# Performance work log

Measured on AMD Instinct MI355X. Metric: run time of the kernel, lower is better.

## Reference

```python
import jax, jax.numpy as jnp
import numpy as np

B, L = 512, 200
WORD_V, PATH_V = 100000, 200000
E, D = 128, 384


def setup_inputs() -> dict:
    key = jax.random.key(0)
    ks = jax.random.split(key, 10)
    inp = {
        "x_s1": jax.random.randint(ks[0], (B, L), 0, WORD_V),
        "path1": jax.random.randint(ks[1], (B, L), 0, PATH_V),
        "x_t1": jax.random.randint(ks[2], (B, L), 0, WORD_V),
        "x_s2": jax.random.randint(ks[3], (B, L), 0, WORD_V),
        "path2": jax.random.randint(ks[4], (B, L), 0, PATH_V),
        "x_t2": jax.random.randint(ks[5], (B, L), 0, WORD_V),
        # learned parameters
        "word_emb": jax.random.normal(ks[6], (WORD_V, E), dtype=jnp.float32) * 0.02,
        "path_emb": jax.random.normal(ks[7], (PATH_V, E), dtype=jnp.float32) * 0.02,
        "W_fc": jax.random.normal(ks[8], (D, 3 * E), dtype=jnp.float32) * (1.0 / np.sqrt(3 * E)),  # nn.Linear weight [out, in], no bias
        "attn": jax.random.uniform(ks[9], (D, 1), dtype=jnp.float32),
    }
    return inp


def _extract(xs, path, xt, word_emb, path_emb, W_fc, attn):
    # gather + concat -> [B, L, 3E]
    ctx = jnp.concatenate([word_emb[xs], path_emb[path], word_emb[xt]], axis=-1)
    # linear (no bias, dropout is identity at eval) + tanh -> [B, L, D]
    h = jnp.tanh(jnp.einsum('blf,df->bld', ctx, W_fc))
    # attention scores [B, L, 1]; the zeros mask in the original is a no-op
    scores = jnp.einsum('bld,do->blo', h, attn)
    a = jax.nn.softmax(scores, axis=1)
    code_vec = jnp.sum(h * a, axis=1)  # [B, D]
    return code_vec, a


def reference(x_s1, path1, x_t1, x_s2, path2, x_t2, word_emb, path_emb, W_fc, attn):
    cv1, _ = _extract(x_s1, path1, x_t1, word_emb, path_emb, W_fc, attn)
    cv2, _ = _extract(x_s2, path2, x_t2, word_emb, path_emb, W_fc, attn)
    return (cv1, cv2)
```

## Files before the change

kernel.cpp:

```cpp
#include <hip/hip_runtime.h>
#include <hip/hip_bf16.h>

#define B_N   512
#define L_N   200
#define E_N   128
#define D_N   384
#define K_N   384
#define M_PAD 208
#define MT_N  13
#define NT_W  3
#define NWAVE 8
#define KSTEP 12
#define STR   136

typedef __bf16 v8bf  __attribute__((ext_vector_type(8)));
typedef float  v4f   __attribute__((ext_vector_type(4)));
typedef unsigned int v4u __attribute__((ext_vector_type(4)));

__device__ __forceinline__ unsigned short f2bf(float f) {
    union { __bf16 b; unsigned short u; } cv;
    cv.b = (__bf16)f;
    return cv.u;
}

__device__ __forceinline__ float fast_tanh(float x) {
    float e = __expf(2.f * x);
    return 1.f - 2.f / (e + 1.f);
}

__global__ void pack_w(const float* __restrict__ W, unsigned short* __restrict__ Wp) {
    int gid  = blockIdx.x * 256 + threadIdx.x;
    int lane = gid & 63;
    int u    = gid >> 6;
    int nt   = u % 3;
    int wv   = (u / 3) & 7;
    int kk   = u / 24;
    int c    = lane & 15;
    int quad = lane >> 4;
    int n    = wv * 48 + nt * 16 + c;
    int k0   = kk * 32 + quad * 8;
    const float* src = W + n * K_N + k0;
    ushort4 lo, hi;
    lo.x = f2bf(src[0]); lo.y = f2bf(src[1]); lo.z = f2bf(src[2]); lo.w = f2bf(src[3]);
    hi.x = f2bf(src[4]); hi.y = f2bf(src[5]); hi.z = f2bf(src[6]); hi.w = f2bf(src[7]);
    ushort4* dst = (ushort4*)(Wp + (size_t)gid * 8);
    dst[0] = lo;
    dst[1] = hi;
}

__global__ __launch_bounds__(512, 2)
void code2vec_fused(const int* __restrict__ xs1, const int* __restrict__ ph1,
                    const int* __restrict__ xt1,
                    const int* __restrict__ xs2, const int* __restrict__ ph2,
                    const int* __restrict__ xt2,
                    const float* __restrict__ wemb, const float* __restrict__ pemb,
                    const unsigned short* __restrict__ Wp,
                    const float* __restrict__ attn,
                    float* __restrict__ out)
{
    const int tid  = threadIdx.x;
    const int wv   = tid >> 6;
    const int lane = tid & 63;
    const int quad = lane >> 4;
    const int c    = lane & 15;
    const int b    = blockIdx.x;
    const int pass = blockIdx.y;

    const int* xs = pass ? xs2 : xs1;
    const int* ph = pass ? ph2 : ph1;
    const int* xt = pass ? xt2 : xt1;

    __shared__ unsigned short Alds[M_PAD * STR];
    __shared__ float sp[NWAVE][M_PAD];
    __shared__ float alds[M_PAD];
    __shared__ int   ilds[3 * L_N];

    if (tid < L_N) {
        ilds[tid]           = xs[b * L_N + tid];
        ilds[L_N + tid]     = ph[b * L_N + tid];
        ilds[2 * L_N + tid] = xt[b * L_N + tid];
    }

    v4f acc[MT_N][NT_W];
    #pragma unroll
    for (int i = 0; i < MT_N; ++i)
        #pragma unroll
        for (int j = 0; j < NT_W; ++j)
            acc[i][j] = (v4f){0.f, 0.f, 0.f, 0.f};

    const v4u* wp4 = (const v4u*)Wp;

    for (int seg = 0; seg < 3; ++seg) {
        const float* ebase = (seg == 1) ? pemb : wemb;
        const int*   idxp  = &ilds[seg * L_N];

        __syncthreads();

        #pragma unroll
        for (int i = 0; i < 7; ++i) {
            int u = i * 512 + tid;
            if (u < M_PAD * 16) {
                int m = u >> 4, jj = u & 15;
                ushort4 lo, hi;
                if (m < L_N) {
                    const float* src = ebase + (size_t)idxp[m] * E_N + jj * 8;
                    const float4 f0 = *(const float4*)(src);
                    const float4 f1 = *(const float4*)(src + 4);
                    lo.x = f2bf(f0.x); lo.y = f2bf(f0.y); lo.z = f2bf(f0.z); lo.w = f2bf(f0.w);
                    hi.x = f2bf(f1.x); hi.y = f2bf(f1.y); hi.z = f2bf(f1.z); hi.w = f2bf(f1.w);
                } else {
                    lo.x = lo.y = lo.z = lo.w = 0;
                    hi.x = hi.y = hi.z = hi.w = 0;
                }
                ushort4* dst = (ushort4*)&Alds[m * STR + jj * 8];
                dst[0] = lo;
                dst[1] = hi;
            }
        }
        __syncthreads();

        #pragma unroll
        for (int t = 0; t < 4; ++t) {
            const int kk = seg * 4 + t;
            v8bf bfrag[NT_W];
            #pragma unroll
            for (int nt = 0; nt < NT_W; ++nt) {
                v4u raw = wp4[((kk * NWAVE + wv) * NT_W + nt) * 64 + lane];
                bfrag[nt] = __builtin_bit_cast(v8bf, raw);
            }
            #pragma unroll
            for (int mt = 0; mt < MT_N; ++mt) {
                v8bf afrag = *(const v8bf*)&Alds[(mt * 16 + c) * STR + t * 32 + quad * 8];
                #pragma unroll
                for (int nt = 0; nt < NT_W; ++nt)
                    acc[mt][nt] = __builtin_amdgcn_mfma_f32_16x16x32_bf16(afrag, bfrag[nt], acc[mt][nt], 0, 0, 0);
            }
        }
    }

    float an[NT_W];
    #pragma unroll
    for (int nt = 0; nt < NT_W; ++nt) an[nt] = attn[wv * 48 + nt * 16 + c];

    #pragma unroll
    for (int mt = 0; mt < MT_N; ++mt) {
        #pragma unroll
        for (int r = 0; r < 4; ++r) {
            float sv = 0.f;
            #pragma unroll
            for (int nt = 0; nt < NT_W; ++nt) {
                float h = fast_tanh(acc[mt][nt][r]);
                acc[mt][nt][r] = h;
                sv += h * an[nt];
            }
            sv += __shfl_xor(sv, 1);
            sv += __shfl_xor(sv, 2);
            sv += __shfl_xor(sv, 4);
            sv += __shfl_xor(sv, 8);
            if (c == 0) sp[wv][mt * 16 + quad * 4 + r] = sv;
        }
    }
    __syncthreads();

    if (tid < M_PAD) {
        float s = 0.f;
        #pragma unroll
        for (int w2 = 0; w2 < NWAVE; ++w2) s += sp[w2][tid];
        alds[tid] = s;
    }
    __syncthreads();

    if (wv == 0) {
        float v0 = alds[lane];
        float v1 = alds[64 + lane];
        float v2 = alds[128 + lane];
        bool  has3 = (192 + lane) < L_N;
        float v3 = has3 ? alds[192 + lane] : -1e30f;
        float mx = fmaxf(fmaxf(v0, v1), fmaxf(v2, v3));
        #pragma unroll
        for (int off = 32; off > 0; off >>= 1) mx = fmaxf(mx, __shfl_xor(mx, off));
        float e0 = __expf(v0 - mx);
        float e1 = __expf(v1 - mx);
        float e2 = __expf(v2 - mx);
        float e3 = has3 ? __expf(v3 - mx) : 0.f;
        float z = e0 + e1 + e2 + e3;
        #pragma unroll
        for (int off = 32; off > 0; off >>= 1) z += __shfl_xor(z, off);
        float inv = 1.f / z;
        alds[lane]       = e0 * inv;
        alds[64 + lane]  = e1 * inv;
        alds[128 + lane] = e2 * inv;
        if (192 + lane < M_PAD) alds[192 + lane] = e3 * inv;
    }
    __syncthreads();

    float* outp = out + (size_t)pass * B_N * D_N + (size_t)b * D_N;
    #pragma unroll
    for (int nt = 0; nt < NT_W; ++nt) {
        float cv = 0.f;
        #pragma unroll
        for (int mt = 0; mt < MT_N; ++mt) {
            #pragma unroll
            for (int r = 0; r < 4; ++r)
                cv += alds[mt * 16 + quad * 4 + r] * acc[mt][nt][r];
        }
        cv += __shfl_xor(cv, 16);
        cv += __shfl_xor(cv, 32);
        if (quad == 0) outp[wv * 48 + nt * 16 + c] = cv;
    }
}

extern "C" void kernel_launch(void* const* d_in, const int* in_sizes, int n_in,
                              void* d_out, int out_size, void* d_ws, size_t ws_size,
                              hipStream_t stream) {
    unsigned short* Wp = (unsigned short*)d_ws;
    pack_w<<<72, 256, 0, stream>>>((const float*)d_in[8], Wp);
    dim3 grid(B_N, 2, 1);
    code2vec_fused<<<grid, 512, 0, stream>>>(
        (const int*)d_in[0], (const int*)d_in[1], (const int*)d_in[2],
        (const int*)d_in[3], (const int*)d_in[4], (const int*)d_in[5],
        (const float*)d_in[6], (const float*)d_in[7],
        Wp, (const float*)d_in[9],
        (float*)d_out);
}
```

Baseline: 358.8 us.

## Split sequence into row chunks with online softmax to cut registers and LDS

The fused kernel now processes the 200 positions in three chunks (80/64/64 rows) instead of holding all 13 M-tiles of accumulators at once. It uses a flash-style running max/sum softmax to combine the chunks. This shrinks per-thread accumulators and the LDS tile, so launch bounds can rise to 4 blocks per CU for more occupancy. The cost is three extra gather/GEMM passes with more barriers, and the W fragments are reloaded for each chunk.

Result: slower. 386.9 us (+7.8%).

```diff
diff --git a/kernel.cpp b/kernel.cpp
--- a/kernel.cpp
+++ b/kernel.cpp
@@ -1,17 +1,12 @@
 #include <hip/hip_runtime.h>
 #include <hip/hip_bf16.h>
 
-#define B_N   512
-#define L_N   200
-#define E_N   128
-#define D_N   384
-#define K_N   384
-#define M_PAD 208
-#define MT_N  13
-#define NT_W  3
-#define NWAVE 8
-#define KSTEP 12
-#define STR   136
+#define B_N 512
+#define L_N 200
+#define E_N 128
+#define D_N 384
+#define K_N 384
+#define STR 136
 
 typedef __bf16 v8bf  __attribute__((ext_vector_type(8)));
 typedef float  v4f   __attribute__((ext_vector_type(4)));
@@ -22,7 +17,6 @@
     cv.b = (__bf16)f;
     return cv.u;
 }
-
 __device__ __forceinline__ float fast_tanh(float x) {
     float e = __expf(2.f * x);
     return 1.f - 2.f / (e + 1.f);
@@ -32,31 +26,26 @@
     int gid  = blockIdx.x * 256 + threadIdx.x;
     int lane = gid & 63;
     int u    = gid >> 6;
-    int nt   = u % 3;
-    int wv   = (u / 3) & 7;
+    int gn   = u % 24;
     int kk   = u / 24;
-    int c    = lane & 15;
-    int quad = lane >> 4;
-    int n    = wv * 48 + nt * 16 + c;
-    int k0   = kk * 32 + quad * 8;
-    const float* src = W + n * K_N + k0;
+    int c    = lane & 15, quad = lane >> 4;
+    const float* src = W + (gn * 16 + c) * K_N + kk * 32 + quad * 8;
     ushort4 lo, hi;
     lo.x = f2bf(src[0]); lo.y = f2bf(src[1]); lo.z = f2bf(src[2]); lo.w = f2bf(src[3]);
     hi.x = f2bf(src[4]); hi.y = f2bf(src[5]); hi.z = f2bf(src[6]); hi.w = f2bf(src[7]);
     ushort4* dst = (ushort4*)(Wp + (size_t)gid * 8);
-    dst[0] = lo;
-    dst[1] = hi;
-}
-
-__global__ __launch_bounds__(512, 2)
-void code2vec_fused(const int* __restrict__ xs1, const int* __restrict__ ph1,
-                    const int* __restrict__ xt1,
-                    const int* __restrict__ xs2, const int* __restrict__ ph2,
-                    const int* __restrict__ xt2,
-                    const float* __restrict__ wemb, const float* __restrict__ pemb,
-                    const unsigned short* __restrict__ Wp,
-                    const float* __restrict__ attn,
-                    float* __restrict__ out)
+    dst[0] = lo; dst[1] = hi;
+}
+
+__global__ __launch_bounds__(512, 4)
+void c2v_fused(const int* __restrict__ xs1, const int* __restrict__ ph1,
+               const int* __restrict__ xt1,
+               const int* __restrict__ xs2, const int* __restrict__ ph2,
+               const int* __restrict__ xt2,
+               const float* __restrict__ wemb, const float* __restrict__ pemb,
+               const unsigned short* __restrict__ Wp,
+               const float* __restrict__ attn,
+               float* __restrict__ out)
 {
     const int tid  = threadIdx.x;
     const int wv   = tid >> 6;
@@ -70,40 +59,49 @@
     const int* ph = pass ? ph2 : ph1;
     const int* xt = pass ? xt2 : xt1;
 
-    __shared__ unsigned short Alds[M_PAD * STR];
-    __shared__ float sp[NWAVE][M_PAD];
-    __shared__ float alds[M_PAD];
-    __shared__ int   ilds[3 * L_N];
-
-    if (tid < L_N) {
-        ilds[tid]           = xs[b * L_N + tid];
-        ilds[L_N + tid]     = ph[b * L_N + tid];
-        ilds[2 * L_N + tid] = xt[b * L_N + tid];
+    __shared__ unsigned short Alds[80 * STR];
+    __shared__ float sp[8][80];
+    __shared__ float alds[130];
+    __shared__ int   ilds[3 * 208];
+
+    for (int u = tid; u < 624; u += 512) {
+        int s = u / 208, g = u - s * 208;
+        const int* tab = (s == 0) ? xs : (s == 1) ? ph : xt;
+        ilds[u] = (g < L_N) ? tab[b * L_N + g] : 0;
     }
 
-    v4f acc[MT_N][NT_W];
-    #pragma unroll
-    for (int i = 0; i < MT_N; ++i)
+    const float an0 = attn[(wv * 3 + 0) * 16 + c];
+    const float an1 = attn[(wv * 3 + 1) * 16 + c];
+    const float an2 = attn[(wv * 3 + 2) * 16 + c];
+
+    float o0 = 0.f, o1 = 0.f, o2 = 0.f;
+    float Mrun = -1e30f, Zrun = 0.f;
+
+    const v4u* wp4 = (const v4u*)Wp;
+
+    for (int chunk = 0; chunk < 3; ++chunk) {
+        const int mtn  = (chunk == 0) ? 5 : 4;
+        const int row0 = (chunk == 0) ? 0 : (16 + 64 * chunk);
+        const int rows = mtn * 16;
+
+        v4f acc[5][3];
         #pragma unroll
-        for (int j = 0; j < NT_W; ++j)
-            acc[i][j] = (v4f){0.f, 0.f, 0.f, 0.f};
-
-    const v4u* wp4 = (const v4u*)Wp;
-
-    for (int seg = 0; seg < 3; ++seg) {
-        const float* ebase = (seg == 1) ? pemb : wemb;
-        const int*   idxp  = &ilds[seg * L_N];
-
-        __syncthreads();
-
-        #pragma unroll
-        for (int i = 0; i < 7; ++i) {
-            int u = i * 512 + tid;
-            if (u < M_PAD * 16) {
+        for (int i = 0; i < 5; ++i)
+            #pragma unroll
+            for (int j = 0; j < 3; ++j)
+                acc[i][j] = (v4f){0.f, 0.f, 0.f, 0.f};
+
+        for (int seg = 0; seg < 3; ++seg) {
+            const float* ebase = (seg == 1) ? pemb : wemb;
+            const int units = rows * 16;
+
+            __syncthreads();
+            for (int u = tid; u < units; u += 512) {
                 int m = u >> 4, jj = u & 15;
+                int g = row0 + m;
                 ushort4 lo, hi;
-                if (m < L_N) {
-                    const float* src = ebase + (size_t)idxp[m] * E_N + jj * 8;
+                if (g < L_N) {
+                    const float* src = ebase + (size_t)ilds[seg * 208 + g] * E_N + jj * 8;
                     const float4 f0 = *(const float4*)(src);
                     const float4 f1 = *(const float4*)(src + 4);
                     lo.x = f2bf(f0.x); lo.y = f2bf(f0.y); lo.z = f2bf(f0.z); lo.w = f2bf(f0.w);
@@ -113,100 +111,106 @@
                     hi.x = hi.y = hi.z = hi.w = 0;
                 }
                 ushort4* dst = (ushort4*)&Alds[m * STR + jj * 8];
-                dst[0] = lo;
-                dst[1] = hi;
+                dst[0] = lo; dst[1] = hi;
+            }
+            __syncthreads();
+
+            for (int t = 0; t < 4; ++t) {
+                const int kk = seg * 4 + t;
+                v8bf b0 = __builtin_bit_cast(v8bf, wp4[(kk * 24 + wv * 3 + 0) * 64 + lane]);
+                v8bf b1 = __builtin_bit_cast(v8bf, wp4[(kk * 24 + wv * 3 + 1) * 64 + lane]);
+                v8bf b2 = __builtin_bit_cast(v8bf, wp4[(kk * 24 + wv * 3 + 2) * 64 + lane]);
+                #pragma unroll
+                for (int mt = 0; mt < 5; ++mt) {
+                    if (mt < mtn) {
+                        v8bf a = *(const v8bf*)&Alds[(mt * 16 + c) * STR + t * 32 + quad * 8];
+                        acc[mt][0] = __builtin_amdgcn_mfma_f32_16x16x32_bf16(a, b0, acc[mt][0], 0, 0, 0);
+                        acc[mt][1] = __builtin_amdgcn_mfma_f32_16x16x32_bf16(a, b1, acc[mt][1], 0, 0, 0);
+                        acc[mt][2] = __builtin_amdgcn_mfma_f32_16x16x32_bf16(a, b2, acc[mt][2], 0, 0, 0);
+                    }
+                }
+            }
+        }
+
+        #pragma unroll
+        for (int mt = 0; mt < 5; ++mt) {
+            if (mt < mtn) {
+                #pragma unroll
+                for (int r = 0; r < 4; ++r) {
+                    float h0 = fast_tanh(acc[mt][0][r]);
+                    float h1 = fast_tanh(acc[mt][1][r]);
+                    float h2 = fast_tanh(acc[mt][2][r]);
+                    acc[mt][0][r] = h0; acc[mt][1][r] = h1; acc[mt][2][r] = h2;
+                    float sv = h0 * an0 + h1 * an1 + h2 * an2;
+                    sv += __shfl_xor(sv, 1);
+                    sv += __shfl_xor(sv, 2);
+                    sv += __shfl_xor(sv, 4);
+                    sv += __shfl_xor(sv, 8);
+                    if (c == 0) sp[wv][mt * 16 + quad * 4 + r] = sv;
+                }
             }
         }
         __syncthreads();
 
+        if (wv == 0) {
+            float s0 = sp[0][lane] + sp[1][lane] + sp[2][lane] + sp[3][lane]
+                     + sp[4][lane] + sp[5][lane] + sp[6][lane] + sp[7][lane];
+            if (row0 + lane >= L_N) s0 = -1e30f;
+            float s1 = -1e30f;
+            if (chunk == 0 && lane < 16) {
+                int j = 64 + lane;
+                s1 = sp[0][j] + sp[1][j] + sp[2][j] + sp[3][j]
+                   + sp[4][j] + sp[5][j] + sp[6][j] + sp[7][j];
+            }
+            float mx = fmaxf(s0, s1);
+            #pragma unroll
+            for (int off = 32; off > 0; off >>= 1) mx = fmaxf(mx, __shfl_xor(mx, off));
+            float Mnew  = fmaxf(Mrun, mx);
+            float alpha = __expf(Mrun - Mnew);
+            float e0 = (s0 > -1e29f) ? __expf(s0 - Mnew) : 0.f;
+            float e1 = (s1 > -1e29f) ? __expf(s1 - Mnew) : 0.f;
+            float zc = e0 + e1;
+            #pragma unroll
+            for (int off = 32; off > 0; off >>= 1) zc += __shfl_xor(zc, off);
+            Zrun = Zrun * alpha + zc;
+            Mrun = Mnew;
+            alds[lane] = e0;
+            alds[64 + lane] = e1;
+            if (lane == 0) alds[128] = alpha;
+        }
+        __syncthreads();
+
+        const float al = alds[128];
+        float p0 = 0.f, p1 = 0.f, p2 = 0.f;
         #pragma unroll
-        for (int t = 0; t < 4; ++t) {
-            const int kk = seg * 4 + t;
-            v8bf bfrag[NT_W];
-            #pragma unroll
-            for (int nt = 0; nt < NT_W; ++nt) {
-                v4u raw = wp4[((kk * NWAVE + wv) * NT_W + nt) * 64 + lane];
-                bfrag[nt] = __builtin_bit_cast(v8bf, raw);
-            }
-            #pragma unroll
-            for (int mt = 0; mt < MT_N; ++mt) {
-                v8bf afrag = *(const v8bf*)&Alds[(mt * 16 + c) * STR + t * 32 + quad * 8];
+        for (int mt = 0; mt < 5; ++mt) {
+            if (mt < mtn) {
                 #pragma unroll
-                for (int nt = 0; nt < NT_W; ++nt)
-                    acc[mt][nt] = __builtin_amdgcn_mfma_f32_16x16x32_bf16(afrag, bfrag[nt], acc[mt][nt], 0, 0, 0);
-            }
-        }
+                for (int r = 0; r < 4; ++r) {
+                    float w = alds[mt * 16 + quad * 4 + r];
+                    p0 += w * acc[mt][0][r];
+                    p1 += w * acc[mt][1][r];
+                    p2 += w * acc[mt][2][r];
+                }
+            }
+        }
+        o0 = o0 * al + p0;
+        o1 = o1 * al + p1;
+        o2 = o2 * al + p2;
     }
 
-    float an[NT_W];
-    #pragma unroll
-    for (int nt = 0; nt < NT_W; ++nt) an[nt] = attn[wv * 48 + nt * 16 + c];
-
-    #pragma unroll
-    for (int mt = 0; mt < MT_N; ++mt) {
-        #pragma unroll
-        for (int r = 0; r < 4; ++r) {
-            float sv = 0.f;
-            #pragma unroll
-            for (int nt = 0; nt < NT_W; ++nt) {
-                float h = fast_tanh(acc[mt][nt][r]);
-                acc[mt][nt][r] = h;
-                sv += h * an[nt];
-            }
-            sv += __shfl_xor(sv, 1);
-            sv += __shfl_xor(sv, 2);
-            sv += __shfl_xor(sv, 4);
-            sv += __shfl_xor(sv, 8);
-            if (c == 0) sp[wv][mt * 16 + quad * 4 + r] = sv;
-        }
-    }
+    if (tid == 0) alds[129] = Zrun;
     __syncthreads();
-
-    if (tid < M_PAD) {
-        float s = 0.f;
-        #pragma unroll
-        for (int w2 = 0; w2 < NWAVE; ++w2) s += sp[w2][tid];
-        alds[tid] = s;
-    }
-    __syncthreads();
-
-    if (wv == 0) {
-        float v0 = alds[lane];
-        float v1 = alds[64 + lane];
-        float v2 = alds[128 + lane];
-        bool  has3 = (192 + lane) < L_N;
-        float v3 = has3 ? alds[192 + lane] : -1e30f;
-        float mx = fmaxf(fmaxf(v0, v1), fmaxf(v2, v3));
-        #pragma unroll
-        for (int off = 32; off > 0; off >>= 1) mx = fmaxf(mx, __shfl_xor(mx, off));
-        float e0 = __expf(v0 - mx);
-        float e1 = __expf(v1 - mx);
-        float e2 = __expf(v2 - mx);
-        float e3 = has3 ? __expf(v3 - mx) : 0.f;
-        float z = e0 + e1 + e2 + e3;
-        #pragma unroll
-        for (int off = 32; off > 0; off >>= 1) z += __shfl_xor(z, off);
-        float inv = 1.f / z;
-        alds[lane]       = e0 * inv;
-        alds[64 + lane]  = e1 * inv;
-        alds[128 + lane] = e2 * inv;
-        if (192 + lane < M_PAD) alds[192 + lane] = e3 * inv;
-    }
-    __syncthreads();
-
-    float* outp = out + (size_t)pass * B_N * D_N + (size_t)b * D_N;
-    #pragma unroll
-    for (int nt = 0; nt < NT_W; ++nt) {
-        float cv = 0.f;
-        #pragma unroll
-        for (int mt = 0; mt < MT_N; ++mt) {
-            #pragma unroll
-            for (int r = 0; r < 4; ++r)
-                cv += alds[mt * 16 + quad * 4 + r] * acc[mt][nt][r];
-        }
-        cv += __shfl_xor(cv, 16);
-        cv += __shfl_xor(cv, 32);
-        if (quad == 0) outp[wv * 48 + nt * 16 + c] = cv;
+    const float zinv = 1.f / alds[129];
+
+    float* outp = out + (size_t)(pass * B_N + b) * D_N;
+    o0 += __shfl_xor(o0, 16); o0 += __shfl_xor(o0, 32);
+    o1 += __shfl_xor(o1, 16); o1 += __shfl_xor(o1, 32);
+    o2 += __shfl_xor(o2, 16); o2 += __shfl_xor(o2, 32);
+    if (quad == 0) {
+        outp[(wv * 3 + 0) * 16 + c] = o0 * zinv;
+        outp[(wv * 3 + 1) * 16 + c] = o1 * zinv;
+        outp[(wv * 3 + 2) * 16 + c] = o2 * zinv;
     }
 }
 
@@ -216,7 +220,7 @@
     unsigned short* Wp = (unsigned short*)d_ws;
     pack_w<<<72, 256, 0, stream>>>((const float*)d_in[8], Wp);
     dim3 grid(B_N, 2, 1);
-    code2vec_fused<<<grid, 512, 0, stream>>>(
+    c2v_fused<<<grid, 512, 0, stream>>>(
         (const int*)d_in[0], (const int*)d_in[1], (const int*)d_in[2],
         (const int*)d_in[3], (const int*)d_in[4], (const int*)d_in[5],
         (const float*)d_in[6], (const float*)d_in[7],
```
